# Kernel tuning notes

Hardware: AMD Instinct MI355X
Metric: run time of the kernel (lower is better)

## Reference

```python
import jax, jax.numpy as jnp
import numpy as np

DMODEL = 2048
NUM_HEADS = 16
NUM_KV_HEADS = 4
HEAD_DIM = DMODEL // NUM_HEADS  # 128
THETA = 10000.0


def setup_inputs() -> dict:
    key = jax.random.key(0)
    k0, k1, k2, k3, k4 = jax.random.split(key, 5)
    B, S = 1, 4096
    x = jax.random.normal(k0, (B, S, DMODEL), dtype=jnp.float32)
    # Linear weights stored as [in, out] (equivalent to torch [out,in] with x @ W.T)
    sd = 0.02
    wq = jax.random.normal(k1, (DMODEL, NUM_HEADS * HEAD_DIM), dtype=jnp.float32) * sd
    wk = jax.random.normal(k2, (DMODEL, NUM_KV_HEADS * HEAD_DIM), dtype=jnp.float32) * sd
    wv = jax.random.normal(k3, (DMODEL, NUM_KV_HEADS * HEAD_DIM), dtype=jnp.float32) * sd
    wo = jax.random.normal(k4, (NUM_HEADS * HEAD_DIM, DMODEL), dtype=jnp.float32) * sd
    return {"x": x, "wq": wq, "wk": wk, "wv": wv, "wo": wo}


def _rope_cos_sin(seqlen, dtype):
    # RoPE.forward: inv_freq over half the head dim, emb = cat(freqs, freqs)
    inv_freq = 1.0 / (THETA ** (jnp.arange(0, HEAD_DIM, 2, dtype=jnp.float32) / HEAD_DIM))
    pos = jnp.arange(seqlen, dtype=jnp.float32)
    freqs = pos[:, None] * inv_freq[None, :]          # [S, HEAD_DIM/2]
    emb = jnp.concatenate([freqs, freqs], axis=-1)    # [S, HEAD_DIM]
    return emb.astype(dtype) * 0 + jnp.cos(emb).astype(dtype), jnp.sin(emb).astype(dtype)


def _rot(t):
    half = t.shape[-1] // 2
    return jnp.concatenate([-t[..., half:], t[..., :half]], axis=-1)


def reference(x, wq, wk, wv, wo):
    B, S, _ = x.shape
    q = (x @ wq).reshape(B, S, NUM_HEADS, HEAD_DIM).transpose(0, 2, 1, 3)      # [B,H,S,D]
    k = (x @ wk).reshape(B, S, NUM_KV_HEADS, HEAD_DIM).transpose(0, 2, 1, 3)   # [B,KV,S,D]
    v = (x @ wv).reshape(B, S, NUM_KV_HEADS, HEAD_DIM).transpose(0, 2, 1, 3)

    cos, sin = _rope_cos_sin(S, x.dtype)  # [S, D]
    cos = cos[None, None, :, :]
    sin = sin[None, None, :, :]
    q = q * cos + _rot(q) * sin
    k = k * cos + _rot(k) * sin

    rep = NUM_HEADS // NUM_KV_HEADS
    k = jnp.repeat(k, rep, axis=1)  # [B,H,S,D]
    v = jnp.repeat(v, rep, axis=1)

    scale = 1.0 / jnp.sqrt(jnp.asarray(HEAD_DIM, dtype=x.dtype))
    scores = jnp.einsum('bhqd,bhkd->bhqk', q, k) * scale
    causal = jnp.tril(jnp.ones((S, S), dtype=bool))
    scores = jnp.where(causal[None, None], scores, jnp.finfo(x.dtype).min)
    attn = jax.nn.softmax(scores, axis=-1)
    o = jnp.einsum('bhqk,bhkd->bhqd', attn, v)          # [B,H,S,D]
    o = o.transpose(0, 2, 1, 3).reshape(B, S, NUM_HEADS * HEAD_DIM)
    return o @ wo
```

## Files before the change

kernel.cpp:

```cpp
#include <hip/hip_runtime.h>
#include <math.h>

#define SEQ   4096
#define DM    2048
#define NH    16
#define NKV   4
#define HD    128
#define QKVN  3072
#define CEXP  0.12753643f

typedef _Float16 f16;
typedef _Float16 f16x8 __attribute__((ext_vector_type(8)));
typedef _Float16 f16x4v __attribute__((ext_vector_type(4)));
typedef float    f32x4 __attribute__((ext_vector_type(4)));

#define GLD16(g, l) __builtin_amdgcn_global_load_lds(                        \
    (const __attribute__((address_space(1))) unsigned int*)(g),              \
    (__attribute__((address_space(3))) unsigned int*)(l), 16, 0, 0)

__global__ __launch_bounds__(256) void cast_f32_f16_k(const float* __restrict__ in,
                                                      f16* __restrict__ out, int n4)
{
    int i = blockIdx.x * 256 + threadIdx.x;
    if (i >= n4) return;
    float4 v = ((const float4*)in)[i];
    f16x4v h = {(f16)v.x, (f16)v.y, (f16)v.z, (f16)v.w};
    ((f16x4v*)out)[i] = h;
}

__global__ __launch_bounds__(256) void transpose_cast_k(const float* __restrict__ in,
                                                        f16* __restrict__ out,
                                                        int R, int Cn, float scale)
{
    __shared__ float tile[32][33];
    int bx = blockIdx.x * 32, by = blockIdx.y * 32;
    int tx = threadIdx.x & 31, ty = threadIdx.x >> 5;
    #pragma unroll
    for (int i = 0; i < 32; i += 8)
        tile[ty + i][tx] = in[(size_t)(by + ty + i) * Cn + bx + tx];
    __syncthreads();
    #pragma unroll
    for (int i = 0; i < 32; i += 8)
        out[(size_t)(bx + ty + i) * R + by + tx] = (f16)(tile[tx][ty + i] * scale);
}

__global__ __launch_bounds__(256) void transpose_f16_k(const f16* __restrict__ in,
                                                       f16* __restrict__ out,
                                                       int R, int Cn, int ldin)
{
    __shared__ f16 tile[32][33];
    int bx = blockIdx.x * 32, by = blockIdx.y * 32;
    int tx = threadIdx.x & 31, ty = threadIdx.x >> 5;
    #pragma unroll
    for (int i = 0; i < 32; i += 8)
        tile[ty + i][tx] = in[(size_t)(by + ty + i) * ldin + bx + tx];
    __syncthreads();
    #pragma unroll
    for (int i = 0; i < 32; i += 8)
        out[(size_t)(bx + ty + i) * R + by + tx] = tile[tx][ty + i];
}

template <int BN, typename OutT>
__global__ __launch_bounds__(512, 2) void gemm8p(const f16* __restrict__ A,
                                                 const f16* __restrict__ Bt,
                                                 OutT* __restrict__ C,
                                                 int M, int N, int K)
{
    constexpr int LB  = (BN == 256) ? 2 : 1;
    constexpr int NF  = BN / 16;
    constexpr int NPP = NF / 4;
    (void)M;

    __shared__ __align__(16) f16 sm[32768 + 2 * BN * 64];
    f16* As = sm;
    f16* Bs = sm + 32768;

    const int t = threadIdx.x;
    const int w = t >> 6;
    const int lane = t & 63, ln = lane & 15, quad = lane >> 4;
    const size_t bm = (size_t)blockIdx.y * 256, bn = (size_t)blockIdx.x * BN;

    auto stageA = [&](int half, int nb, size_t kn) {
        #pragma unroll
        for (int cc = 0; cc < 2; ++cc) {
            int pos = cc * 512 + t;
            int rl  = pos >> 3;
            int sc  = (pos & 7) ^ (rl & 7);
            GLD16(A + (bm + half * 128 + rl) * (size_t)K + kn + sc * 8,
                  As + nb * 16384 + half * 8192 + pos * 8);
        }
    };
    auto stageB = [&](int half, int nb, size_t kn) {
        #pragma unroll
        for (int cc = 0; cc < LB; ++cc) {
            int pos = cc * 512 + t;
            int rl  = pos >> 3;
            int sc  = (pos & 7) ^ (rl & 7);
            GLD16(Bt + (bn + half * (BN / 2) + rl) * (size_t)K + kn + sc * 8,
                  Bs + nb * (BN * 64) + half * (BN * 32) + pos * 8);
        }
    };

    f32x4 acc[2][NF];
    #pragma unroll
    for (int i = 0; i < 2; ++i)
        #pragma unroll
        for (int j = 0; j < NF; ++j) acc[i][j] = (f32x4){0.f, 0.f, 0.f, 0.f};

    const int KT = K >> 6;

    stageA(0, 0, 0); stageA(1, 0, 0); stageB(0, 0, 0); stageB(1, 0, 0);
    asm volatile("s_waitcnt vmcnt(0)" ::: "memory");
    __builtin_amdgcn_s_barrier();

    f16x8 af[2][2];

    for (int kt = 0; kt < KT; ++kt) {
        const int b = kt & 1, nb = b ^ 1;
        const size_t kn = (size_t)((kt + 1 < KT) ? (kt + 1) * 64 : (KT - 1) * 64);
        const int Ab = b * 16384, Bb = b * (BN * 64);

        #pragma unroll
        for (int q = 0; q < 4; ++q) {
            if (q == 0) {
                #pragma unroll
                for (int i = 0; i < 2; ++i)
                    #pragma unroll
                    for (int kk = 0; kk < 2; ++kk)
                        af[i][kk] = *(const f16x8*)&As[Ab + (w * 32 + i * 16 + ln) * 64
                                                         + ((kk * 4 + quad) ^ (ln & 7)) * 8];
            }
            f16x8 bf[NPP][2];
            #pragma unroll
            for (int jj = 0; jj < NPP; ++jj)
                #pragma unroll
                for (int kk = 0; kk < 2; ++kk)
                    bf[jj][kk] = *(const f16x8*)&Bs[Bb + ((q * NPP + jj) * 16 + ln) * 64
                                                       + ((kk * 4 + quad) ^ (ln & 7)) * 8];

            if (q == 0) stageA(0, nb, kn);
            if (q == 1) stageA(1, nb, kn);
            if (q == 2) stageB(0, nb, kn);
            if (q == 3) stageB(1, nb, kn);

            if (q == 1) asm volatile("s_waitcnt vmcnt(4)" ::: "memory");
            if (q == 3) {
                if constexpr (LB == 2) asm volatile("s_waitcnt vmcnt(2)" ::: "memory");
                else                   asm volatile("s_waitcnt vmcnt(1)" ::: "memory");
            }

            __builtin_amdgcn_sched_barrier(0);
            __builtin_amdgcn_s_barrier();
            __builtin_amdgcn_sched_barrier(0);
            __builtin_amdgcn_s_setprio(1);
            #pragma unroll
            for (int jj = 0; jj < NPP; ++jj)
                #pragma unroll
                for (int i = 0; i < 2; ++i)
                    #pragma unroll
                    for (int kk = 0; kk < 2; ++kk)
                        acc[i][q * NPP + jj] = __builtin_amdgcn_mfma_f32_16x16x32_f16(
                            af[i][kk], bf[jj][kk], acc[i][q * NPP + jj], 0, 0, 0);
            __builtin_amdgcn_s_setprio(0);
            __builtin_amdgcn_sched_barrier(0);
        }
    }

    #pragma unroll
    for (int i = 0; i < 2; ++i)
        #pragma unroll
        for (int j = 0; j < NF; ++j)
            #pragma unroll
            for (int r = 0; r < 4; ++r)
                C[(bm + w * 32 + i * 16 + quad * 4 + r) * (size_t)N + bn + j * 16 + ln]
                    = (OutT)acc[i][j][r];
}

__global__ __launch_bounds__(256) void rope_k(f16* __restrict__ qkv)
{
    const int s = blockIdx.x, t = threadIdx.x;
    for (int p = t; p < (NH + NKV) * 64; p += 256) {
        int hh = p >> 6, i = p & 63;
        f16* base = (hh < NH) ? qkv + (size_t)s * QKVN + hh * HD
                              : qkv + (size_t)s * QKVN + DM + (hh - NH) * HD;
        float inv = __builtin_exp2f((float)i * -0.20762050f);
        float ang = (float)s * inv;
        float c = cosf(ang), sn = sinf(ang);
        float x0 = (float)base[i], x1 = (float)base[i + 64];
        base[i]      = (f16)(x0 * c - x1 * sn);
        base[i + 64] = (f16)(x1 * c + x0 * sn);
    }
}

__global__ __launch_bounds__(256, 2) void flash_k(const f16* __restrict__ qkv,
                                                  const f16* __restrict__ vt,
                                                  f16* __restrict__ O0,
                                                  f16* __restrict__ O1,
                                                  float* __restrict__ lpart)
{
    const int bid  = blockIdx.x;
    const int xcd  = bid & 7;
    const int rr   = bid >> 3;
    const int kvh  = xcd >> 1;
    const int h    = kvh * 4 + (xcd & 1) * 2 + (rr & 1);
    const int px   = (rr >> 1) & 15;
    const int half = rr >> 5;

    const int t = threadIdx.x, w = t >> 6, lane = t & 63, ln = lane & 15, quad = lane >> 4;

    f16*   Op = half ? O1 : O0;
    float* lp = lpart + (size_t)half * NH * SEQ + (size_t)h * SEQ;

    __shared__ __align__(16) f16 sm[40960];
    f16* Ps = sm + 32768 + w * 2048;

    const int glo = half * 33;
    const int ghi = glo + 33;

    int krow[4], kc[4], vrow[4], vc[4];
    #pragma unroll
    for (int cc = 0; cc < 4; ++cc) {
        int pos = cc * 256 + t;
        krow[cc] = pos >> 4; kc[cc] = (pos & 15) ^ (krow[cc] & 15);
        vrow[cc] = pos >> 3; vc[cc] = (pos & 7) ^ (vrow[cc] & 7);
    }

    #pragma unroll
    for (int ph = 0; ph < 2; ++ph) {
        const int bx   = ph ? (31 - px) : px;
        const int q0   = bx * 128;
        const int ntp  = 2 * bx + 2;
        const int base = ph ? (2 * px + 2) : 0;
        int tb_lo = glo - base; if (tb_lo < 0) tb_lo = 0;
        int tb_hi = ghi - base; if (tb_hi > ntp) tb_hi = ntp;

        const f16* kp[4]; const f16* vp[4];
        #pragma unroll
        for (int cc = 0; cc < 4; ++cc) {
            kp[cc] = qkv + (size_t)(tb_lo * 64 + krow[cc]) * QKVN + DM + kvh * HD + kc[cc] * 8;
            vp[cc] = vt  + (size_t)(kvh * HD + vrow[cc]) * SEQ + tb_lo * 64 + vc[cc] * 8;
        }
        auto stage = [&](int b) {
            f16* Kd = sm + b * 8192;
            f16* Vd = sm + 16384 + b * 8192;
            #pragma unroll
            for (int cc = 0; cc < 4; ++cc) {
                GLD16(kp[cc], Kd + (cc * 256 + t) * 8);
                GLD16(vp[cc], Vd + (cc * 256 + t) * 8);
                kp[cc] += 64 * QKVN;
                vp[cc] += 64;
            }
        };

        f16x8 qf[2][4];
        #pragma unroll
        for (int rf = 0; rf < 2; ++rf) {
            const f16* qrow = qkv + (size_t)(q0 + w * 32 + rf * 16 + ln) * QKVN + h * HD;
            #pragma unroll
            for (int tt = 0; tt < 4; ++tt)
                qf[rf][tt] = *(const f16x8*)(qrow + tt * 32 + quad * 8);
        }

        float l_r[2][4] = {{0.f, 0.f, 0.f, 0.f}, {0.f, 0.f, 0.f, 0.f}};
        f32x4 oacc[2][8];
        #pragma unroll
        for (int rf = 0; rf < 2; ++rf)
            #pragma unroll
            for (int dt = 0; dt < 8; ++dt) oacc[rf][dt] = (f32x4){0.f, 0.f, 0.f, 0.f};

        if (tb_lo < tb_hi) stage(0);
        __syncthreads();

        for (int tb = tb_lo; tb < tb_hi; ++tb) {
            const int cur = (tb - tb_lo) & 1;
            if (tb + 1 < tb_hi) stage(cur ^ 1);

            const f16* Ks  = sm + cur * 8192;
            const f16* Vts = sm + 16384 + cur * 8192;

            f32x4 sacc[2][4];
            #pragma unroll
            for (int rf = 0; rf < 2; ++rf)
                #pragma unroll
                for (int c2 = 0; c2 < 4; ++c2) sacc[rf][c2] = (f32x4){0.f, 0.f, 0.f, 0.f};
            #pragma unroll
            for (int tt = 0; tt < 4; ++tt) {
                #pragma unroll
                for (int c2 = 0; c2 < 4; ++c2) {
                    f16x8 bk = *(const f16x8*)&Ks[(c2 * 16 + ln) * 128 + ((tt * 4 + quad) ^ ln) * 8];
                    sacc[0][c2] = __builtin_amdgcn_mfma_f32_16x16x32_f16(qf[0][tt], bk, sacc[0][c2], 0, 0, 0);
                    sacc[1][c2] = __builtin_amdgcn_mfma_f32_16x16x32_f16(qf[1][tt], bk, sacc[1][c2], 0, 0, 0);
                }
            }

            if (tb >= ntp - 2) {
                const int ko = (tb - (ntp - 2)) * 64;
                #pragma unroll
                for (int rf = 0; rf < 2; ++rf)
                    #pragma unroll
                    for (int c2 = 0; c2 < 4; ++c2)
                        #pragma unroll
                        for (int r = 0; r < 4; ++r)
                            if (ko + c2 * 16 + ln > w * 32 + rf * 16 + quad * 4 + r)
                                sacc[rf][c2][r] = -INFINITY;
            }

            #pragma unroll
            for (int rf = 0; rf < 2; ++rf)
                #pragma unroll
                for (int c2 = 0; c2 < 4; ++c2)
                    #pragma unroll
                    for (int r = 0; r < 4; ++r) {
                        float e = __builtin_exp2f(sacc[rf][c2][r]);
                        l_r[rf][r] += e;
                        int row = rf * 16 + quad * 4 + r;
                        int slot = (c2 * 2 + (ln >> 3)) ^ (row & 7);
                        Ps[row * 64 + slot * 8 + (ln & 7)] = (f16)e;
                    }

            #pragma unroll
            for (int t2 = 0; t2 < 2; ++t2) {
                f16x8 pa0 = *(const f16x8*)&Ps[(0 * 16 + ln) * 64 + ((t2 * 4 + quad) ^ (ln & 7)) * 8];
                f16x8 pa1 = *(const f16x8*)&Ps[(1 * 16 + ln) * 64 + ((t2 * 4 + quad) ^ (ln & 7)) * 8];
                #pragma unroll
                for (int dt = 0; dt < 8; ++dt) {
                    f16x8 bv = *(const f16x8*)&Vts[(dt * 16 + ln) * 64 + ((t2 * 4 + quad) ^ (ln & 7)) * 8];
                    oacc[0][dt] = __builtin_amdgcn_mfma_f32_16x16x32_f16(pa0, bv, oacc[0][dt], 0, 0, 0);
                    oacc[1][dt] = __builtin_amdgcn_mfma_f32_16x16x32_f16(pa1, bv, oacc[1][dt], 0, 0, 0);
                }
            }

            __syncthreads();
        }

        #pragma unroll
        for (int rf = 0; rf < 2; ++rf)
            #pragma unroll
            for (int r = 0; r < 4; ++r) {
                float l = l_r[rf][r];
                l += __shfl_xor(l, 1, 64);
                l += __shfl_xor(l, 2, 64);
                l += __shfl_xor(l, 4, 64);
                l += __shfl_xor(l, 8, 64);
                if (ln == 0)
                    lp[q0 + w * 32 + rf * 16 + quad * 4 + r] = l;
            }
        #pragma unroll
        for (int rf = 0; rf < 2; ++rf)
            #pragma unroll
            for (int dt = 0; dt < 8; ++dt)
                #pragma unroll
                for (int r = 0; r < 4; ++r)
                    Op[(size_t)(q0 + w * 32 + rf * 16 + quad * 4 + r) * DM + h * HD + dt * 16 + ln]
                        = (f16)oacc[rf][dt][r];
    }
}

__global__ __launch_bounds__(256) void merge_k(const f16* __restrict__ O0,
                                               const f16* __restrict__ O1,
                                               const float* __restrict__ l0,
                                               const float* __restrict__ l1,
                                               f16* __restrict__ oh)
{
    int idx = blockIdx.x * 256 + threadIdx.x;
    int row = idx >> 8;
    int hh  = (idx & 255) >> 4;
    float li = 1.0f / (l0[hh * SEQ + row] + l1[hh * SEQ + row]);
    f16x8 a = ((const f16x8*)O0)[idx];
    f16x8 b = ((const f16x8*)O1)[idx];
    f16x8 o;
    #pragma unroll
    for (int i = 0; i < 8; ++i)
        o[i] = (f16)(((float)a[i] + (float)b[i]) * li);
    ((f16x8*)oh)[idx] = o;
}

extern "C" void kernel_launch(void* const* d_in, const int* in_sizes, int n_in,
                              void* d_out, int out_size, void* d_ws, size_t ws_size,
                              hipStream_t stream)
{
    (void)in_sizes; (void)n_in; (void)out_size; (void)ws_size;
    const float* x  = (const float*)d_in[0];
    const float* wq = (const float*)d_in[1];
    const float* wk = (const float*)d_in[2];
    const float* wv = (const float*)d_in[3];
    const float* wo = (const float*)d_in[4];
    float* out = (float*)d_out;

    f16* xh    = (f16*)d_ws;
    f16* wtqkv = xh + 8388608ull;
    f16* wot   = wtqkv + 6291456ull;
    f16* qkvb  = wot + 4194304ull;
    f16* vtb   = qkvb + 12582912ull;
    f16* O1    = vtb + 2097152ull;
    f16* O0    = xh;
    f16* oh    = xh;
    float* lbuf = (float*)wtqkv;

    cast_f32_f16_k<<<8192, 256, 0, stream>>>(x, xh, 2097152);
    transpose_cast_k<<<dim3(64, 64), 256, 0, stream>>>(wq, wtqkv, 2048, 2048, CEXP);
    transpose_cast_k<<<dim3(16, 64), 256, 0, stream>>>(wk, wtqkv + 2048ull * 2048, 2048, 512, 1.0f);
    transpose_cast_k<<<dim3(16, 64), 256, 0, stream>>>(wv, wtqkv + 2560ull * 2048, 2048, 512, 1.0f);
    transpose_cast_k<<<dim3(64, 64), 256, 0, stream>>>(wo, wot, 2048, 2048, 1.0f);

    gemm8p<256, f16><<<dim3(12, 16), 512, 0, stream>>>(xh, wtqkv, qkvb, 4096, 3072, 2048);
    rope_k<<<4096, 256, 0, stream>>>(qkvb);
    transpose_f16_k<<<dim3(16, 128), 256, 0, stream>>>(qkvb + 2560, vtb, 4096, 512, 3072);
    flash_k<<<dim3(512), 256, 0, stream>>>(qkvb, vtb, O0, O1, lbuf);
    merge_k<<<4096, 256, 0, stream>>>(O0, O1, lbuf, lbuf + (size_t)NH * SEQ, oh);
    gemm8p<128, float><<<dim3(16, 16), 512, 0, stream>>>(oh, wot, out, 4096, 2048, 2048);
}
```

Measured before the change: 327.6 us.

## Split flash attention block across 8 waves with 16 query rows each

The flash attention kernel now launches 512 threads (8 waves) per block, and each wave owns 16 query rows instead of 32, so per-thread accumulator and Q-fragment registers are halved. K/V tile staging is spread over twice as many threads, and the per-wave P scratch shrinks so the total LDS footprint stays the same. The aim is more waves in flight for latency hiding. In exchange, each K/V fragment read from LDS feeds half as many MFMAs, which raises LDS traffic per FLOP, and the larger block may make synchronisation costlier.

```diff
diff --git a/kernel.cpp b/kernel.cpp
--- a/kernel.cpp
+++ b/kernel.cpp
@@ -192,7 +192,7 @@
     }
 }
 
-__global__ __launch_bounds__(256, 2) void flash_k(const f16* __restrict__ qkv,
+__global__ __launch_bounds__(512, 4) void flash_k(const f16* __restrict__ qkv,
                                                   const f16* __restrict__ vt,
                                                   f16* __restrict__ O0,
                                                   f16* __restrict__ O1,
@@ -212,15 +212,15 @@
     float* lp = lpart + (size_t)half * NH * SEQ + (size_t)h * SEQ;
 
     __shared__ __align__(16) f16 sm[40960];
-    f16* Ps = sm + 32768 + w * 2048;
+    f16* Ps = sm + 32768 + w * 1024;
 
     const int glo = half * 33;
     const int ghi = glo + 33;
 
-    int krow[4], kc[4], vrow[4], vc[4];
-    #pragma unroll
-    for (int cc = 0; cc < 4; ++cc) {
-        int pos = cc * 256 + t;
+    int krow[2], kc[2], vrow[2], vc[2];
+    #pragma unroll
+    for (int cc = 0; cc < 2; ++cc) {
+        int pos = cc * 512 + t;
         krow[cc] = pos >> 4; kc[cc] = (pos & 15) ^ (krow[cc] & 15);
         vrow[cc] = pos >> 3; vc[cc] = (pos & 7) ^ (vrow[cc] & 7);
     }
@@ -234,9 +234,9 @@
         int tb_lo = glo - base; if (tb_lo < 0) tb_lo = 0;
         int tb_hi = ghi - base; if (tb_hi > ntp) tb_hi = ntp;
 
-        const f16* kp[4]; const f16* vp[4];
-        #pragma unroll
-        for (int cc = 0; cc < 4; ++cc) {
+        const f16* kp[2]; const f16* vp[2];
+        #pragma unroll
+        for (int cc = 0; cc < 2; ++cc) {
             kp[cc] = qkv + (size_t)(tb_lo * 64 + krow[cc]) * QKVN + DM + kvh * HD + kc[cc] * 8;
             vp[cc] = vt  + (size_t)(kvh * HD + vrow[cc]) * SEQ + tb_lo * 64 + vc[cc] * 8;
         }
@@ -244,29 +244,26 @@
             f16* Kd = sm + b * 8192;
             f16* Vd = sm + 16384 + b * 8192;
             #pragma unroll
-            for (int cc = 0; cc < 4; ++cc) {
-                GLD16(kp[cc], Kd + (cc * 256 + t) * 8);
-                GLD16(vp[cc], Vd + (cc * 256 + t) * 8);
+            for (int cc = 0; cc < 2; ++cc) {
+                GLD16(kp[cc], Kd + (cc * 512 + t) * 8);
+                GLD16(vp[cc], Vd + (cc * 512 + t) * 8);
                 kp[cc] += 64 * QKVN;
                 vp[cc] += 64;
             }
         };
 
-        f16x8 qf[2][4];
-        #pragma unroll
-        for (int rf = 0; rf < 2; ++rf) {
-            const f16* qrow = qkv + (size_t)(q0 + w * 32 + rf * 16 + ln) * QKVN + h * HD;
+        f16x8 qf[4];
+        {
+            const f16* qrow = qkv + (size_t)(q0 + w * 16 + ln) * QKVN + h * HD;
             #pragma unroll
             for (int tt = 0; tt < 4; ++tt)
-                qf[rf][tt] = *(const f16x8*)(qrow + tt * 32 + quad * 8);
-        }
-
-        float l_r[2][4] = {{0.f, 0.f, 0.f, 0.f}, {0.f, 0.f, 0.f, 0.f}};
-        f32x4 oacc[2][8];
-        #pragma unroll
-        for (int rf = 0; rf < 2; ++rf)
-            #pragma unroll
-            for (int dt = 0; dt < 8; ++dt) oacc[rf][dt] = (f32x4){0.f, 0.f, 0.f, 0.f};
+                qf[tt] = *(const f16x8*)(qrow + tt * 32 + quad * 8);
+        }
+
+        float l_r[4] = {0.f, 0.f, 0.f, 0.f};
+        f32x4 oacc[8];
+        #pragma unroll
+        for (int dt = 0; dt < 8; ++dt) oacc[dt] = (f32x4){0.f, 0.f, 0.f, 0.f};
 
         if (tb_lo < tb_hi) stage(0);
         __syncthreads();
@@ -277,56 +274,47 @@
 
             const f16* Ks  = sm + cur * 8192;
             const f16* Vts = sm + 16384 + cur * 8192;
-
-            f32x4 sacc[2][4];
-            #pragma unroll
-            for (int rf = 0; rf < 2; ++rf)
-                #pragma unroll
-                for (int c2 = 0; c2 < 4; ++c2) sacc[rf][c2] = (f32x4){0.f, 0.f, 0.f, 0.f};
-            #pragma unroll
-            for (int tt = 0; tt < 4; ++tt) {
+            const bool diag = (tb >= ntp - 2);
+            const int  ko   = diag ? (tb - (ntp - 2)) * 64 : 0;
+
+            f32x4 sacc[4];
+            #pragma unroll
+            for (int c2 = 0; c2 < 4; ++c2) sacc[c2] = (f32x4){0.f, 0.f, 0.f, 0.f};
+            #pragma unroll
+            for (int tt = 0; tt < 4; ++tt)
                 #pragma unroll
                 for (int c2 = 0; c2 < 4; ++c2) {
                     f16x8 bk = *(const f16x8*)&Ks[(c2 * 16 + ln) * 128 + ((tt * 4 + quad) ^ ln) * 8];
-                    sacc[0][c2] = __builtin_amdgcn_mfma_f32_16x16x32_f16(qf[0][tt], bk, sacc[0][c2], 0, 0, 0);
-                    sacc[1][c2] = __builtin_amdgcn_mfma_f32_16x16x32_f16(qf[1][tt], bk, sacc[1][c2], 0, 0, 0);
+                    sacc[c2] = __builtin_amdgcn_mfma_f32_16x16x32_f16(qf[tt], bk, sacc[c2], 0, 0, 0);
                 }
-            }
-
-            if (tb >= ntp - 2) {
-                const int ko = (tb - (ntp - 2)) * 64;
-                #pragma unroll
-                for (int rf = 0; rf < 2; ++rf)
-                    #pragma unroll
-                    for (int c2 = 0; c2 < 4; ++c2)
-                        #pragma unroll
-                        for (int r = 0; r < 4; ++r)
-                            if (ko + c2 * 16 + ln > w * 32 + rf * 16 + quad * 4 + r)
-                                sacc[rf][c2][r] = -INFINITY;
-            }
-
-            #pragma unroll
-            for (int rf = 0; rf < 2; ++rf)
+
+            if (diag) {
                 #pragma unroll
                 for (int c2 = 0; c2 < 4; ++c2)
                     #pragma unroll
-                    for (int r = 0; r < 4; ++r) {
-                        float e = __builtin_exp2f(sacc[rf][c2][r]);
-                        l_r[rf][r] += e;
-                        int row = rf * 16 + quad * 4 + r;
-                        int slot = (c2 * 2 + (ln >> 3)) ^ (row & 7);
-                        Ps[row * 64 + slot * 8 + (ln & 7)] = (f16)e;
-                    }
+                    for (int r = 0; r < 4; ++r)
+                        if (ko + c2 * 16 + ln > w * 16 + quad * 4 + r)
+                            sacc[c2][r] = -INFINITY;
+            }
+
+            #pragma unroll
+            for (int c2 = 0; c2 < 4; ++c2)
+                #pragma unroll
+                for (int r = 0; r < 4; ++r) {
+                    float e = __builtin_exp2f(sacc[c2][r]);
+                    l_r[r] += e;
+                    int row = quad * 4 + r;
+                    int slot = (c2 * 2 + (ln >> 3)) ^ (row & 7);
+                    Ps[row * 64 + slot * 8 + (ln & 7)] = (f16)e;
+                }
 
             #pragma unroll
             for (int t2 = 0; t2 < 2; ++t2) {
-                f16x8 pa0 = *(const f16x8*)&Ps[(0 * 16 + ln) * 64 + ((t2 * 4 + quad) ^ (ln & 7)) * 8];
-                f16x8 pa1 = *(const f16x8*)&Ps[(1 * 16 + ln) * 64 + ((t2 * 4 + quad) ^ (ln & 7)) * 8];
+                f16x8 pa = *(const f16x8*)&Ps[ln * 64 + ((t2 * 4 + quad) ^ (ln & 7)) * 8];
                 #pragma unroll
                 for (int dt = 0; dt < 8; ++dt) {
                     f16x8 bv = *(const f16x8*)&Vts[(dt * 16 + ln) * 64 + ((t2 * 4 + quad) ^ (ln & 7)) * 8];
-                    oacc[0][dt] = __builtin_amdgcn_mfma_f32_16x16x32_f16(pa0, bv, oacc[0][dt], 0, 0, 0);
-                    oacc[1][dt] = __builtin_amdgcn_mfma_f32_16x16x32_f16(pa1, bv, oacc[1][dt], 0, 0, 0);
+                    oacc[dt] = __builtin_amdgcn_mfma_f32_16x16x32_f16(pa, bv, oacc[dt], 0, 0, 0);
                 }
             }
 
@@ -334,25 +322,21 @@
         }
 
         #pragma unroll
-        for (int rf = 0; rf < 2; ++rf)
-            #pragma unroll
-            for (int r = 0; r < 4; ++r) {
-                float l = l_r[rf][r];
-                l += __shfl_xor(l, 1, 64);
-                l += __shfl_xor(l, 2, 64);
-                l += __shfl_xor(l, 4, 64);
-                l += __shfl_xor(l, 8, 64);
-                if (ln == 0)
-                    lp[q0 + w * 32 + rf * 16 + quad * 4 + r] = l;
-            }
-        #pragma unroll
-        for (int rf = 0; rf < 2; ++rf)
-            #pragma unroll
-            for (int dt = 0; dt < 8; ++dt)
-                #pragma unroll
-                for (int r = 0; r < 4; ++r)
-                    Op[(size_t)(q0 + w * 32 + rf * 16 + quad * 4 + r) * DM + h * HD + dt * 16 + ln]
-                        = (f16)oacc[rf][dt][r];
+        for (int r = 0; r < 4; ++r) {
+            float l = l_r[r];
+            l += __shfl_xor(l, 1, 64);
+            l += __shfl_xor(l, 2, 64);
+            l += __shfl_xor(l, 4, 64);
+            l += __shfl_xor(l, 8, 64);
+            if (ln == 0)
+                lp[q0 + w * 16 + quad * 4 + r] = l;
+        }
+        #pragma unroll
+        for (int dt = 0; dt < 8; ++dt)
+            #pragma unroll
+            for (int r = 0; r < 4; ++r)
+                Op[(size_t)(q0 + w * 16 + quad * 4 + r) * DM + h * HD + dt * 16 + ln]
+                    = (f16)oacc[dt][r];
     }
 }
 
@@ -406,7 +390,7 @@
     gemm8p<256, f16><<<dim3(12, 16), 512, 0, stream>>>(xh, wtqkv, qkvb, 4096, 3072, 2048);
     rope_k<<<4096, 256, 0, stream>>>(qkvb);
     transpose_f16_k<<<dim3(16, 128), 256, 0, stream>>>(qkvb + 2560, vtb, 4096, 512, 3072);
-    flash_k<<<dim3(512), 256, 0, stream>>>(qkvb, vtb, O0, O1, lbuf);
+    flash_k<<<dim3(512), 512, 0, stream>>>(qkvb, vtb, O0, O1, lbuf);
     merge_k<<<4096, 256, 0, stream>>>(O0, O1, lbuf, lbuf + (size_t)NH * SEQ, oh);
     gemm8p<128, float><<<dim3(16, 16), 512, 0, stream>>>(oh, wot, out, 4096, 2048, 2048);
 }
```

Result: slower. 340.2 us (+3.8%).

## Double flash-attention query tile to 256 rows per block, halving grid

Applied to the files above, without the earlier changes.

Each wave now handles 64 query rows instead of 32, so a block covers 256 queries and reuses every staged K/V tile for twice as many rows. The grid drops from 512 to 256 blocks, and the pairing and split bounds are adjusted to match (16 tile pairs, 34 KV tiles per half). Launch bounds fall to one block per SIMD to fit the doubled accumulators. The aim is to halve K/V global and LDS traffic per unit of work, at the cost of lower occupancy, fewer blocks than the chip has CUs, and coarser load balance across the causal triangle.

```diff
diff --git a/kernel.cpp b/kernel.cpp
--- a/kernel.cpp
+++ b/kernel.cpp
@@ -192,7 +192,7 @@
     }
 }
 
-__global__ __launch_bounds__(256, 2) void flash_k(const f16* __restrict__ qkv,
+__global__ __launch_bounds__(256, 1) void flash_k(const f16* __restrict__ qkv,
                                                   const f16* __restrict__ vt,
                                                   f16* __restrict__ O0,
                                                   f16* __restrict__ O1,
@@ -203,19 +203,19 @@
     const int rr   = bid >> 3;
     const int kvh  = xcd >> 1;
     const int h    = kvh * 4 + (xcd & 1) * 2 + (rr & 1);
-    const int px   = (rr >> 1) & 15;
-    const int half = rr >> 5;
+    const int px   = (rr >> 1) & 7;
+    const int half = rr >> 4;
 
     const int t = threadIdx.x, w = t >> 6, lane = t & 63, ln = lane & 15, quad = lane >> 4;
 
     f16*   Op = half ? O1 : O0;
     float* lp = lpart + (size_t)half * NH * SEQ + (size_t)h * SEQ;
 
-    __shared__ __align__(16) f16 sm[40960];
-    f16* Ps = sm + 32768 + w * 2048;
-
-    const int glo = half * 33;
-    const int ghi = glo + 33;
+    __shared__ __align__(16) f16 sm[49152];
+    f16* Ps = sm + 32768 + w * 4096;
+
+    const int glo = half * 34;
+    const int ghi = glo + 34;
 
     int krow[4], kc[4], vrow[4], vc[4];
     #pragma unroll
@@ -227,10 +227,10 @@
 
     #pragma unroll
     for (int ph = 0; ph < 2; ++ph) {
-        const int bx   = ph ? (31 - px) : px;
-        const int q0   = bx * 128;
-        const int ntp  = 2 * bx + 2;
-        const int base = ph ? (2 * px + 2) : 0;
+        const int bx   = ph ? (15 - px) : px;
+        const int q0   = bx * 256;
+        const int ntp  = 4 * bx + 4;
+        const int base = ph ? (4 * px + 4) : 0;
         int tb_lo = glo - base; if (tb_lo < 0) tb_lo = 0;
         int tb_hi = ghi - base; if (tb_hi > ntp) tb_hi = ntp;
 
@@ -252,19 +252,23 @@
             }
         };
 
-        f16x8 qf[2][4];
-        #pragma unroll
-        for (int rf = 0; rf < 2; ++rf) {
-            const f16* qrow = qkv + (size_t)(q0 + w * 32 + rf * 16 + ln) * QKVN + h * HD;
+        f16x8 qf[4][4];
+        #pragma unroll
+        for (int rf = 0; rf < 4; ++rf) {
+            const f16* qrow = qkv + (size_t)(q0 + w * 64 + rf * 16 + ln) * QKVN + h * HD;
             #pragma unroll
             for (int tt = 0; tt < 4; ++tt)
                 qf[rf][tt] = *(const f16x8*)(qrow + tt * 32 + quad * 8);
         }
 
-        float l_r[2][4] = {{0.f, 0.f, 0.f, 0.f}, {0.f, 0.f, 0.f, 0.f}};
-        f32x4 oacc[2][8];
-        #pragma unroll
-        for (int rf = 0; rf < 2; ++rf)
+        float l_r[4][4];
+        #pragma unroll
+        for (int rf = 0; rf < 4; ++rf)
+            #pragma unroll
+            for (int r = 0; r < 4; ++r) l_r[rf][r] = 0.f;
+        f32x4 oacc[4][8];
+        #pragma unroll
+        for (int rf = 0; rf < 4; ++rf)
             #pragma unroll
             for (int dt = 0; dt < 8; ++dt) oacc[rf][dt] = (f32x4){0.f, 0.f, 0.f, 0.f};
 
@@ -277,36 +281,37 @@
 
             const f16* Ks  = sm + cur * 8192;
             const f16* Vts = sm + 16384 + cur * 8192;
-
-            f32x4 sacc[2][4];
-            #pragma unroll
-            for (int rf = 0; rf < 2; ++rf)
+            const bool diag = (tb >= ntp - 4);
+            const int  ko   = diag ? (tb - (ntp - 4)) * 64 : 0;
+
+            f32x4 sacc[4][4];
+            #pragma unroll
+            for (int rf = 0; rf < 4; ++rf)
                 #pragma unroll
                 for (int c2 = 0; c2 < 4; ++c2) sacc[rf][c2] = (f32x4){0.f, 0.f, 0.f, 0.f};
             #pragma unroll
-            for (int tt = 0; tt < 4; ++tt) {
+            for (int tt = 0; tt < 4; ++tt)
                 #pragma unroll
                 for (int c2 = 0; c2 < 4; ++c2) {
                     f16x8 bk = *(const f16x8*)&Ks[(c2 * 16 + ln) * 128 + ((tt * 4 + quad) ^ ln) * 8];
-                    sacc[0][c2] = __builtin_amdgcn_mfma_f32_16x16x32_f16(qf[0][tt], bk, sacc[0][c2], 0, 0, 0);
-                    sacc[1][c2] = __builtin_amdgcn_mfma_f32_16x16x32_f16(qf[1][tt], bk, sacc[1][c2], 0, 0, 0);
+                    #pragma unroll
+                    for (int rf = 0; rf < 4; ++rf)
+                        sacc[rf][c2] = __builtin_amdgcn_mfma_f32_16x16x32_f16(qf[rf][tt], bk, sacc[rf][c2], 0, 0, 0);
                 }
-            }
-
-            if (tb >= ntp - 2) {
-                const int ko = (tb - (ntp - 2)) * 64;
-                #pragma unroll
-                for (int rf = 0; rf < 2; ++rf)
+
+            if (diag) {
+                #pragma unroll
+                for (int rf = 0; rf < 4; ++rf)
                     #pragma unroll
                     for (int c2 = 0; c2 < 4; ++c2)
                         #pragma unroll
                         for (int r = 0; r < 4; ++r)
-                            if (ko + c2 * 16 + ln > w * 32 + rf * 16 + quad * 4 + r)
+                            if (ko + c2 * 16 + ln > w * 64 + rf * 16 + quad * 4 + r)
                                 sacc[rf][c2][r] = -INFINITY;
             }
 
             #pragma unroll
-            for (int rf = 0; rf < 2; ++rf)
+            for (int rf = 0; rf < 4; ++rf)
                 #pragma unroll
                 for (int c2 = 0; c2 < 4; ++c2)
                     #pragma unroll
@@ -320,13 +325,16 @@
 
             #pragma unroll
             for (int t2 = 0; t2 < 2; ++t2) {
-                f16x8 pa0 = *(const f16x8*)&Ps[(0 * 16 + ln) * 64 + ((t2 * 4 + quad) ^ (ln & 7)) * 8];
-                f16x8 pa1 = *(const f16x8*)&Ps[(1 * 16 + ln) * 64 + ((t2 * 4 + quad) ^ (ln & 7)) * 8];
+                f16x8 pa[4];
+                #pragma unroll
+                for (int rf = 0; rf < 4; ++rf)
+                    pa[rf] = *(const f16x8*)&Ps[(rf * 16 + ln) * 64 + ((t2 * 4 + quad) ^ (ln & 7)) * 8];
                 #pragma unroll
                 for (int dt = 0; dt < 8; ++dt) {
                     f16x8 bv = *(const f16x8*)&Vts[(dt * 16 + ln) * 64 + ((t2 * 4 + quad) ^ (ln & 7)) * 8];
-                    oacc[0][dt] = __builtin_amdgcn_mfma_f32_16x16x32_f16(pa0, bv, oacc[0][dt], 0, 0, 0);
-                    oacc[1][dt] = __builtin_amdgcn_mfma_f32_16x16x32_f16(pa1, bv, oacc[1][dt], 0, 0, 0);
+                    #pragma unroll
+                    for (int rf = 0; rf < 4; ++rf)
+                        oacc[rf][dt] = __builtin_amdgcn_mfma_f32_16x16x32_f16(pa[rf], bv, oacc[rf][dt], 0, 0, 0);
                 }
             }
 
@@ -334,7 +342,7 @@
         }
 
         #pragma unroll
-        for (int rf = 0; rf < 2; ++rf)
+        for (int rf = 0; rf < 4; ++rf)
             #pragma unroll
             for (int r = 0; r < 4; ++r) {
                 float l = l_r[rf][r];
@@ -343,15 +351,15 @@
                 l += __shfl_xor(l, 4, 64);
                 l += __shfl_xor(l, 8, 64);
                 if (ln == 0)
-                    lp[q0 + w * 32 + rf * 16 + quad * 4 + r] = l;
-            }
-        #pragma unroll
-        for (int rf = 0; rf < 2; ++rf)
+                    lp[q0 + w * 64 + rf * 16 + quad * 4 + r] = l;
+            }
+        #pragma unroll
+        for (int rf = 0; rf < 4; ++rf)
             #pragma unroll
             for (int dt = 0; dt < 8; ++dt)
                 #pragma unroll
                 for (int r = 0; r < 4; ++r)
-                    Op[(size_t)(q0 + w * 32 + rf * 16 + quad * 4 + r) * DM + h * HD + dt * 16 + ln]
+                    Op[(size_t)(q0 + w * 64 + rf * 16 + quad * 4 + r) * DM + h * HD + dt * 16 + ln]
                         = (f16)oacc[rf][dt][r];
     }
 }
@@ -406,7 +414,7 @@
     gemm8p<256, f16><<<dim3(12, 16), 512, 0, stream>>>(xh, wtqkv, qkvb, 4096, 3072, 2048);
     rope_k<<<4096, 256, 0, stream>>>(qkvb);
     transpose_f16_k<<<dim3(16, 128), 256, 0, stream>>>(qkvb + 2560, vtb, 4096, 512, 3072);
-    flash_k<<<dim3(512), 256, 0, stream>>>(qkvb, vtb, O0, O1, lbuf);
+    flash_k<<<dim3(256), 256, 0, stream>>>(qkvb, vtb, O0, O1, lbuf);
     merge_k<<<4096, 256, 0, stream>>>(O0, O1, lbuf, lbuf + (size_t)NH * SEQ, oh);
     gemm8p<128, float><<<dim3(16, 16), 512, 0, stream>>>(oh, wot, out, 4096, 2048, 2048);
 }
```

Measured after the change: 365.8 us. 11.7% more time.
